# Kernel tuning notes

Measured on AMD Instinct MI355X. Metric: run time of the kernel, lower is better.

## Reference

```python
import jax, jax.numpy as jnp
import numpy as np


def conv1d(x, w, b, pad):
    # x: [N, Cin, L], w: [Cout, Cin, K] (torch OIH layout)
    out = jax.lax.conv_general_dilated(
        x, w, window_strides=(1,), padding=[(pad, pad)],
        dimension_numbers=("NCH", "OIH", "NCH"))
    return out + b[None, :, None]


def adaptive_avg_pool1d(x, out_size):
    # Faithful torch AdaptiveAvgPool1d: bin i covers [floor(i*L/D), ceil((i+1)*L/D))
    L = x.shape[-1]
    i = jnp.arange(out_size)
    starts = (i * L) // out_size
    ends = ((i + 1) * L + out_size - 1) // out_size
    zeros = jnp.zeros(x.shape[:-1] + (1,), dtype=x.dtype)
    cs = jnp.concatenate([zeros, jnp.cumsum(x, axis=-1)], axis=-1)
    counts = (ends - starts).astype(x.dtype)
    return (cs[..., ends] - cs[..., starts]) / counts


def setup_inputs() -> dict:
    key = jax.random.key(0)
    ks = jax.random.split(key, 12)
    B, C, T, D = 16, 64, 1024, 1024  # output_dim must equal seq_len (broadcast in forward)
    s = lambda fan: 1.0 / np.sqrt(fan)
    return {
        "eeg_data": jax.random.normal(ks[0], (B, C, T), jnp.float32),
        "filter_strength": jnp.ones((1,), jnp.float32),
        # spectral_attention params
        "aw1": jax.random.normal(ks[1], (32, 1, 64), jnp.float32) * s(64),
        "ab1": jnp.zeros((32,), jnp.float32),
        "aw2": jax.random.normal(ks[2], (64, 32, 32), jnp.float32) * s(32 * 32),
        "ab2": jnp.zeros((64,), jnp.float32),
        "aw3": jax.random.normal(ks[3], (1, 64, 1), jnp.float32) * s(64),
        "ab3": jnp.zeros((1,), jnp.float32),
        # feature_projection params
        "fw1": jax.random.normal(ks[4], (64, 1, 128), jnp.float32) * s(128),
        "fb1": jnp.zeros((64,), jnp.float32),
        "bn_g": jnp.ones((64,), jnp.float32),
        "bn_b": jnp.zeros((64,), jnp.float32),
        "bn_m": jnp.zeros((64,), jnp.float32),
        "bn_v": jnp.ones((64,), jnp.float32),
        "fw2": jax.random.normal(ks[5], (D, 64, 1), jnp.float32) * s(64),
        "fb2": jnp.zeros((D,), jnp.float32),
    }


def reference(eeg_data, filter_strength, aw1, ab1, aw2, ab2, aw3, ab3,
              fw1, fb1, bn_g, bn_b, bn_m, bn_v, fw2, fb2):
    B, C, T = eeg_data.shape
    D = fw2.shape[0]
    EPS = 1e-5
    # LearnableBandpassFilter: elementwise scale
    filt = eeg_data * filter_strength
    # spectral attention over channel-averaged signal
    ca = jnp.mean(filt, axis=1, keepdims=True)           # [B,1,T]
    a = jax.nn.relu(conv1d(ca, aw1, ab1, 32))            # [B,32,T+1]
    a = jax.nn.relu(conv1d(a, aw2, ab2, 16))             # [B,64,T+2]
    a = adaptive_avg_pool1d(a, D)                        # [B,64,D]
    attn = jax.nn.sigmoid(conv1d(a, aw3, ab3, 0))        # [B,1,D], D==T
    attended = filt * attn                               # [B,C,T]
    # feature_projection: shared weights over channels -> batch the python loop
    x = attended.reshape(B * C, 1, T)
    h = conv1d(x, fw1, fb1, 64)                          # [B*C,64,T+1]
    h = (h - bn_m[None, :, None]) * jax.lax.rsqrt(bn_v[None, :, None] + EPS)
    h = h * bn_g[None, :, None] + bn_b[None, :, None]
    h = jax.nn.relu(h)
    h = adaptive_avg_pool1d(h, D)                        # [B*C,64,D]
    h = conv1d(h, fw2, fb2, 0)                           # [B*C,D,D]
    feats = h.reshape(B, C, D, D).mean(axis=1)           # mean over channels
    return feats, attn[:, 0, :]
```

## Files before the change

### kernel.cpp

```cpp
#include <hip/hip_runtime.h>
#include <math.h>

#define Bn 16
#define Cn 64
#define Tn 1024
#define Dn 1024

#define CA_S   1088
#define CA_OFF 0
#define AT_OFF 17408
#define A2_S   1026
#define A2_OFF 599040
#define XS_U   (2*50176)
#define HS_S   1040
#define HS_OFF 2671616
#define HB_OFF 4801536

#define A1S_U  (2*HS_OFF)
#define HBT_U  (2*HB_OFF)
#define WFW2_U (HBT_U + 1048576)
#define WAW2_U (WFW2_U + 65536)
#define WFW1_U (WAW2_U + 65536)

typedef __attribute__((ext_vector_type(4))) float f32x4;
typedef __attribute__((ext_vector_type(8))) short bf16x8;
typedef __attribute__((ext_vector_type(4))) unsigned int u32x4;

static __device__ inline unsigned short f2bf(float x) {
  unsigned u = __builtin_bit_cast(unsigned, x);
  return (unsigned short)((u + 0x7fffu + ((u >> 16) & 1u)) >> 16);
}

__global__ void kI_init(const float* __restrict__ eeg, const float* __restrict__ fsp,
                        const float* __restrict__ aw2, const float* __restrict__ fw2,
                        const float* __restrict__ fw1, float* __restrict__ ws) {
  int bx = blockIdx.x, tid = threadIdx.x;
  if (bx < 64) {
    int b = bx >> 2, x = bx & 3;
    int t = x * 256 + tid;
    float s = 0.f;
#pragma unroll 8
    for (int c = 0; c < 64; ++c) s += eeg[(b * 64 + c) * 1024 + t];
    ws[CA_OFF + b * CA_S + 32 + t] = s * fsp[0] * (1.f / 64.f);
    if (x == 0 && tid < 32) ws[CA_OFF + b * CA_S + tid] = 0.f;
    if (x == 3 && tid >= 224) ws[CA_OFF + b * CA_S + 1056 + (tid - 224)] = 0.f;
    return;
  }
  int id = (bx - 64) * 256 + tid;
  if (id < 16384) {
    int e0 = id * 4;
    float4 f = *(const float4*)&aw2[e0];
    unsigned short* d = (unsigned short*)ws + WAW2_U + e0;
    d[0] = f2bf(f.x); d[1] = f2bf(f.y); d[2] = f2bf(f.z); d[3] = f2bf(f.w);
  } else if (id < 32768) {
    int e0 = (id - 16384) * 4;
    float4 f = *(const float4*)&fw2[e0];
    unsigned short* d = (unsigned short*)ws + WFW2_U + e0;
    d[0] = f2bf(f.x); d[1] = f2bf(f.y); d[2] = f2bf(f.z); d[3] = f2bf(f.w);
  } else if (id < 34816) {
    int e0 = (id - 32768) * 4;
    float4 f = *(const float4*)&fw1[e0];
    unsigned short* d = (unsigned short*)ws + WFW1_U + e0;
    d[0] = f2bf(f.x); d[1] = f2bf(f.y); d[2] = f2bf(f.z); d[3] = f2bf(f.w);
  }
}

__global__ void k2s_conv1(const float* __restrict__ aw1, const float* __restrict__ ab1,
                          float* __restrict__ ws) {
  int row = blockIdx.x;
  int b = row >> 5, o = row & 31;
  int tid = threadIdx.x;
  __shared__ unsigned short xl[1232];
  for (int i = tid; i < 1232; i += 256)
    if (i < 16 || i >= 1041) xl[i] = 0;
  const float* cab = ws + CA_OFF + b * CA_S;
  float bias = ab1[o];
  for (int t = tid; t < 1025; t += 256) {
    float acc = bias;
#pragma unroll 8
    for (int k = 0; k < 64; ++k) acc += aw1[o * 64 + k] * cab[t + k];
    xl[16 + t] = f2bf(fmaxf(acc, 0.f));
  }
  __syncthreads();
  unsigned short* a1s = (unsigned short*)ws + A1S_U;
  for (int q = tid; q < 608; q += 256) {
    int s = q / 152, mm = q % 152;
    int e = mm * 8;
    unsigned a0 = xl[e + s + 0], a1 = xl[e + s + 1], a2 = xl[e + s + 2], a3 = xl[e + s + 3];
    unsigned a4 = xl[e + s + 4], a5 = xl[e + s + 5], a6 = xl[e + s + 6], a7 = xl[e + s + 7];
    uint4 v;
    v.x = a0 | (a1 << 16); v.y = a2 | (a3 << 16); v.z = a4 | (a5 << 16); v.w = a6 | (a7 << 16);
    *(uint4*)&a1s[(s * 512 + row) * 1216 + e] = v;
  }
}

__global__ __launch_bounds__(256) void k3_mfma(const float* __restrict__ ab2,
                                               float* __restrict__ ws) {
  int t0 = blockIdx.x * 64, b = blockIdx.y, oh = blockIdx.z;
  int tid = threadIdx.x, l = tid & 63, w = tid >> 6;
  __shared__ unsigned short wlds[16 * 1032];
  __shared__ unsigned short xlds[32 * 4 * 104];
  const unsigned short* wb = (const unsigned short*)ws + WAW2_U;
  const unsigned short* a1s = (const unsigned short*)ws + A1S_U;
#pragma unroll
  for (int r = 0; r < 8; ++r) {
    int idx = tid + r * 256;
    int o = idx >> 7, j = idx & 127;
    *(uint4*)&wlds[o * 1032 + j * 8] = *(const uint4*)&wb[(oh * 16 + o) * 1024 + j * 8];
  }
#pragma unroll
  for (int r = 0; r < 6; ++r) {
    int idx = tid + r * 256;
    int i = idx / 48, rem = idx % 48, s = rem / 12, mm = rem % 12;
    *(uint4*)&xlds[(i * 4 + s) * 104 + mm * 8] =
        *(const uint4*)&a1s[(s * 512 + b * 32 + i) * 1216 + t0 + mm * 8];
  }
  __syncthreads();
  int m = l & 15, q = l >> 4;
  int A0 = w * 16 + m + q * 8;
  int xoffb = (A0 & 3) * 104 + (A0 & ~3);
  f32x4 acc = (f32x4){0.f, 0.f, 0.f, 0.f};
  for (int i = 0; i < 32; ++i) {
    const uint2* p = (const uint2*)&xlds[i * 416 + xoffb];
    uint2 lo = p[0], hi = p[1];
    u32x4 bb; bb.x = lo.x; bb.y = lo.y; bb.z = hi.x; bb.w = hi.y;
    u32x4 a = *(const u32x4*)&wlds[m * 1032 + i * 32 + q * 8];
    acc = __builtin_amdgcn_mfma_f32_16x16x32_bf16(
        __builtin_bit_cast(bf16x8, a), __builtin_bit_cast(bf16x8, bb), acc, 0, 0, 0);
  }
  int t = t0 + w * 16 + m;
  if (t < 1026) {
#pragma unroll
    for (int r = 0; r < 4; ++r) {
      int o = oh * 16 + q * 4 + r;
      ws[A2_OFF + (b * 64 + o) * A2_S + t] = fmaxf(acc[r] + ab2[o], 0.f);
    }
  }
}

__global__ void k4_attn(const float* __restrict__ aw3, const float* __restrict__ ab3,
                        float* __restrict__ ws, float* __restrict__ out) {
  int b = blockIdx.y, t = blockIdx.x * 256 + threadIdx.x;
  int s = t + (t >= 512 ? 1 : 0);
  float acc = 0.f;
#pragma unroll 8
  for (int i = 0; i < 64; ++i) {
    const float* row = ws + A2_OFF + (b * 64 + i) * A2_S;
    acc += aw3[i] * (row[s] + row[s + 1]);
  }
  float a = 1.f / (1.f + expf(-(acc * 0.5f + ab3[0])));
  ws[AT_OFF + b * 1024 + t] = a;
  out[16777216 + b * 1024 + t] = a;
}

__global__ void k4b_xs(const float* __restrict__ eeg, const float* __restrict__ fsp,
                       float* __restrict__ ws) {
  int bc = blockIdx.x;
  int b = bc >> 6;
  int tid = threadIdx.x;
  __shared__ unsigned short xsl[1288];
  float fs = fsp[0];
  for (int i = tid; i < 1288; i += 256) {
    int j = i - 64;
    float v = 0.f;
    if (j >= 0 && j < 1024) v = eeg[bc * 1024 + j] * fs * ws[AT_OFF + b * 1024 + j];
    xsl[i] = f2bf(v);
  }
  __syncthreads();
  unsigned short* xsg = (unsigned short*)ws + XS_U;
  for (int q = tid; q < 640; q += 256) {
    int s = q / 160, m = q % 160, e = m * 8;
    uint4 v;
    unsigned a0 = xsl[e + s + 0], a1 = xsl[e + s + 1], a2 = xsl[e + s + 2], a3 = xsl[e + s + 3];
    unsigned a4 = xsl[e + s + 4], a5 = xsl[e + s + 5], a6 = xsl[e + s + 6], a7 = xsl[e + s + 7];
    v.x = a0 | (a1 << 16); v.y = a2 | (a3 << 16); v.z = a4 | (a5 << 16); v.w = a6 | (a7 << 16);
    *(uint4*)&xsg[(s * 1024 + bc) * 1280 + e] = v;
  }
}

__global__ __launch_bounds__(256, 3) void k5_mfma(
    const float* __restrict__ fb1,
    const float* __restrict__ bng, const float* __restrict__ bnb,
    const float* __restrict__ bnm, const float* __restrict__ bnv,
    float* __restrict__ ws) {
  int t0 = blockIdx.x * 64, b = blockIdx.y, g2 = blockIdx.z;
  int tid = threadIdx.x, l = tid & 63, w = tid >> 6;
  __shared__ unsigned short xlds[32 * 4 * 200];
  const unsigned short* wbf = (const unsigned short*)ws + WFW1_U;
  const unsigned short* xsg = (const unsigned short*)ws + XS_U;
#pragma unroll
  for (int r = 0; r < 12; ++r) {
    int q = tid + r * 256;
    int ch = q / 96, rem = q % 96, s = rem / 24, m = rem % 24;
    int c = g2 * 32 + ch;
    uint4 v = *(const uint4*)&xsg[((s * 1024) + b * 64 + c) * 1280 + t0 + m * 8];
    *(uint4*)&xlds[(ch * 4 + s) * 200 + m * 8] = v;
  }
  u32x4 wf[4][4];
#pragma unroll
  for (int mt = 0; mt < 4; ++mt)
#pragma unroll
    for (int ks = 0; ks < 4; ++ks)
      wf[mt][ks] = *(const u32x4*)&wbf[(mt * 16 + (l & 15)) * 128 + ks * 32 + (l >> 4) * 8];
  int row0 = (l >> 4) * 4;
  float scv[4][4], shv[4][4];
#pragma unroll
  for (int mt = 0; mt < 4; ++mt)
#pragma unroll
    for (int r = 0; r < 4; ++r) {
      int o = mt * 16 + row0 + r;
      float s = bng[o] * rsqrtf(bnv[o] + 1e-5f);
      scv[mt][r] = s;
      shv[mt][r] = (fb1[o] - bnm[o]) * s + bnb[o];
    }
  int xoff[4];
#pragma unroll
  for (int ks = 0; ks < 4; ++ks) {
    int A0 = (l & 15) + ks * 32 + (l >> 4) * 8;
    int s = A0 & 3, e = A0 & ~3;
    xoff[ks] = s * 200 + w * 16 + e;
  }
  __syncthreads();
  f32x4 acc[4];
#pragma unroll
  for (int mt = 0; mt < 4; ++mt) acc[mt] = (f32x4){0.f, 0.f, 0.f, 0.f};
  for (int ch = 0; ch < 32; ++ch) {
    u32x4 bf[4];
#pragma unroll
    for (int ks = 0; ks < 4; ++ks) {
      const uint2* p = (const uint2*)&xlds[ch * 800 + xoff[ks]];
      uint2 lo = p[0], hi = p[1];
      u32x4 bb; bb.x = lo.x; bb.y = lo.y; bb.z = hi.x; bb.w = hi.y;
      bf[ks] = bb;
    }
#pragma unroll
    for (int mt = 0; mt < 4; ++mt) {
      f32x4 c = (f32x4){0.f, 0.f, 0.f, 0.f};
#pragma unroll
      for (int ks = 0; ks < 4; ++ks)
        c = __builtin_amdgcn_mfma_f32_16x16x32_bf16(
            __builtin_bit_cast(bf16x8, wf[mt][ks]),
            __builtin_bit_cast(bf16x8, bf[ks]), c, 0, 0, 0);
#pragma unroll
      for (int r = 0; r < 4; ++r)
        acc[mt][r] += fmaxf(c[r] * scv[mt][r] + shv[mt][r], 0.f);
    }
  }
  int t = t0 + w * 16 + (l & 15);
  if (t < 1025) {
#pragma unroll
    for (int mt = 0; mt < 4; ++mt)
#pragma unroll
      for (int r = 0; r < 4; ++r)
        ws[HS_OFF + (((g2 * 16 + b) * 64) + mt * 16 + row0 + r) * HS_S + t] = acc[mt][r];
  }
}

__global__ void k5b_t(float* __restrict__ ws) {
  int tt = blockIdx.x, b = blockIdx.y;
  int tid = threadIdx.x;
  __shared__ unsigned short tr[64 * 80];
  int k = tid >> 2, q = tid & 3;
  const float* r0 = ws + HS_OFF + ((0 + b) * 64 + k) * HS_S + tt * 64;
  const float* r1 = ws + HS_OFF + ((16 + b) * 64 + k) * HS_S + tt * 64;
#pragma unroll
  for (int j = 0; j < 16; ++j) {
    int tl = q * 16 + j;
    float v = r0[tl] + r0[tl + 1] + r1[tl] + r1[tl + 1];
    tr[tl * 80 + k] = f2bf(v * (1.f / 128.f));
  }
  __syncthreads();
  unsigned short* hbT = (unsigned short*)ws + HBT_U;
#pragma unroll
  for (int r = 0; r < 2; ++r) {
    int idx = tid + r * 256;
    int tl = idx >> 3, j = idx & 7;
    uint4 v = *(uint4*)&tr[tl * 80 + j * 8];
    *(uint4*)&hbT[(b * 1024 + tt * 64 + tl) * 64 + j * 8] = v;
  }
}

__global__ __launch_bounds__(256) void k6_mfma(const float* __restrict__ fb2,
                                               float* __restrict__ ws,
                                               float* __restrict__ out) {
  int tt = blockIdx.x, dt = blockIdx.y, b = blockIdx.z;
  int tid = threadIdx.x, l = tid & 63, w = tid >> 6;
  int wd = w >> 1, wt = w & 1;
  __shared__ unsigned short wA[64 * 80], xB[64 * 80];
  const unsigned short* w2 = (const unsigned short*)ws + WFW2_U;
  const unsigned short* hbT = (const unsigned short*)ws + HBT_U;
#pragma unroll
  for (int r = 0; r < 2; ++r) {
    int idx = tid + r * 256;
    int row = idx >> 3, j = idx & 7;
    *(uint4*)&wA[row * 80 + j * 8] = *(const uint4*)&w2[(dt * 64 + row) * 64 + j * 8];
    *(uint4*)&xB[row * 80 + j * 8] = *(const uint4*)&hbT[(b * 1024 + tt * 64 + row) * 64 + j * 8];
  }
  __syncthreads();
  int m = l & 15, q = l >> 4;
  f32x4 acc[2][2];
#pragma unroll
  for (int mt = 0; mt < 2; ++mt)
#pragma unroll
    for (int nt = 0; nt < 2; ++nt) acc[mt][nt] = (f32x4){0.f, 0.f, 0.f, 0.f};
#pragma unroll
  for (int ks = 0; ks < 2; ++ks) {
    u32x4 a[2], bb[2];
#pragma unroll
    for (int mt = 0; mt < 2; ++mt)
      a[mt] = *(const u32x4*)&wA[(wd * 32 + mt * 16 + m) * 80 + ks * 32 + q * 8];
#pragma unroll
    for (int nt = 0; nt < 2; ++nt)
      bb[nt] = *(const u32x4*)&xB[(wt * 32 + nt * 16 + m) * 80 + ks * 32 + q * 8];
#pragma unroll
    for (int mt = 0; mt < 2; ++mt)
#pragma unroll
      for (int nt = 0; nt < 2; ++nt)
        acc[mt][nt] = __builtin_amdgcn_mfma_f32_16x16x32_bf16(
            __builtin_bit_cast(bf16x8, a[mt]), __builtin_bit_cast(bf16x8, bb[nt]),
            acc[mt][nt], 0, 0, 0);
  }
#pragma unroll
  for (int mt = 0; mt < 2; ++mt) {
#pragma unroll
    for (int r = 0; r < 4; ++r) {
      int d = dt * 64 + wd * 32 + mt * 16 + q * 4 + r;
      float bias = fb2[d];
#pragma unroll
      for (int nt = 0; nt < 2; ++nt) {
        int t = tt * 64 + wt * 32 + nt * 16 + m;
        out[(b * 1024 + d) * 1024 + t] = acc[mt][nt][r] + bias;
      }
    }
  }
}

extern "C" void kernel_launch(void* const* d_in, const int* in_sizes, int n_in,
                              void* d_out, int out_size, void* d_ws, size_t ws_size,
                              hipStream_t stream) {
  const float* eeg = (const float*)d_in[0];
  const float* fsp = (const float*)d_in[1];
  const float* aw1 = (const float*)d_in[2];
  const float* ab1 = (const float*)d_in[3];
  const float* aw2 = (const float*)d_in[4];
  const float* ab2 = (const float*)d_in[5];
  const float* aw3 = (const float*)d_in[6];
  const float* ab3 = (const float*)d_in[7];
  const float* fw1 = (const float*)d_in[8];
  const float* fb1 = (const float*)d_in[9];
  const float* bng = (const float*)d_in[10];
  const float* bnb = (const float*)d_in[11];
  const float* bnm = (const float*)d_in[12];
  const float* bnv = (const float*)d_in[13];
  const float* fw2 = (const float*)d_in[14];
  const float* fb2 = (const float*)d_in[15];
  float* out = (float*)d_out;
  float* ws = (float*)d_ws;

  hipLaunchKernelGGL(kI_init, dim3(200), dim3(256), 0, stream, eeg, fsp, aw2, fw2, fw1, ws);
  hipLaunchKernelGGL(k2s_conv1, dim3(512), dim3(256), 0, stream, aw1, ab1, ws);
  hipLaunchKernelGGL(k3_mfma, dim3(17, 16, 4), dim3(256), 0, stream, ab2, ws);
  hipLaunchKernelGGL(k4_attn, dim3(4, 16), dim3(256), 0, stream, aw3, ab3, ws, out);
  hipLaunchKernelGGL(k4b_xs, dim3(1024), dim3(256), 0, stream, eeg, fsp, ws);
  hipLaunchKernelGGL(k5_mfma, dim3(17, 16, 2), dim3(256), 0, stream,
                     fb1, bng, bnb, bnm, bnv, ws);
  hipLaunchKernelGGL(k5b_t, dim3(16, 16), dim3(256), 0, stream, ws);
  hipLaunchKernelGGL(k6_mfma, dim3(16, 16, 16), dim3(256), 0, stream, fb2, ws, out);
}
```

Baseline: 178.3 us.

## Fuse pooling/transpose into final GEMM kernel and enlarge tiles to 128x128

Removes the separate k5b_t kernel that pooled and transposed the feature projection into bf16. k6_mfma now reads the fp32 hs buffer directly, pools adjacent pairs across the two half-channel partial sums, and writes the transposed bf16 tile into shared memory. The output tile grows from 64x64 to 128x128 per block, with 16 accumulators per wave. This saves one launch and the hbT round trip through memory. In exchange, each hs element is recomputed by the 8 d-tiles, and register pressure rises.

```diff
diff --git a/kernel.cpp b/kernel.cpp
--- a/kernel.cpp
+++ b/kernel.cpp
@@ -256,79 +256,69 @@
   }
 }
 
-__global__ void k5b_t(float* __restrict__ ws) {
-  int tt = blockIdx.x, b = blockIdx.y;
-  int tid = threadIdx.x;
-  __shared__ unsigned short tr[64 * 80];
-  int k = tid >> 2, q = tid & 3;
-  const float* r0 = ws + HS_OFF + ((0 + b) * 64 + k) * HS_S + tt * 64;
-  const float* r1 = ws + HS_OFF + ((16 + b) * 64 + k) * HS_S + tt * 64;
-#pragma unroll
-  for (int j = 0; j < 16; ++j) {
-    int tl = q * 16 + j;
-    float v = r0[tl] + r0[tl + 1] + r1[tl] + r1[tl + 1];
-    tr[tl * 80 + k] = f2bf(v * (1.f / 128.f));
-  }
-  __syncthreads();
-  unsigned short* hbT = (unsigned short*)ws + HBT_U;
-#pragma unroll
-  for (int r = 0; r < 2; ++r) {
-    int idx = tid + r * 256;
-    int tl = idx >> 3, j = idx & 7;
-    uint4 v = *(uint4*)&tr[tl * 80 + j * 8];
-    *(uint4*)&hbT[(b * 1024 + tt * 64 + tl) * 64 + j * 8] = v;
-  }
-}
-
-__global__ __launch_bounds__(256) void k6_mfma(const float* __restrict__ fb2,
-                                               float* __restrict__ ws,
-                                               float* __restrict__ out) {
+__global__ __launch_bounds__(256, 4) void k6_mfma(const float* __restrict__ fb2,
+                                                  float* __restrict__ ws,
+                                                  float* __restrict__ out) {
   int tt = blockIdx.x, dt = blockIdx.y, b = blockIdx.z;
   int tid = threadIdx.x, l = tid & 63, w = tid >> 6;
   int wd = w >> 1, wt = w & 1;
-  __shared__ unsigned short wA[64 * 80], xB[64 * 80];
+  __shared__ unsigned short wA[128 * 72];
+  __shared__ unsigned short xB[128 * 72];
   const unsigned short* w2 = (const unsigned short*)ws + WFW2_U;
-  const unsigned short* hbT = (const unsigned short*)ws + HBT_U;
-#pragma unroll
-  for (int r = 0; r < 2; ++r) {
+#pragma unroll
+  for (int r = 0; r < 4; ++r) {
     int idx = tid + r * 256;
     int row = idx >> 3, j = idx & 7;
-    *(uint4*)&wA[row * 80 + j * 8] = *(const uint4*)&w2[(dt * 64 + row) * 64 + j * 8];
-    *(uint4*)&xB[row * 80 + j * 8] = *(const uint4*)&hbT[(b * 1024 + tt * 64 + row) * 64 + j * 8];
-  }
-  __syncthreads();
-  int m = l & 15, q = l >> 4;
-  f32x4 acc[2][2];
-#pragma unroll
-  for (int mt = 0; mt < 2; ++mt)
-#pragma unroll
-    for (int nt = 0; nt < 2; ++nt) acc[mt][nt] = (f32x4){0.f, 0.f, 0.f, 0.f};
+    *(uint4*)&wA[row * 72 + j * 8] = *(const uint4*)&w2[(dt * 128 + row) * 64 + j * 8];
+  }
+  {
+    int k = tid >> 2, q = tid & 3;
+    const float* r0 = ws + HS_OFF + ((0 + b) * 64 + k) * HS_S + tt * 128 + q * 32;
+    const float* r1 = ws + HS_OFF + ((16 + b) * 64 + k) * HS_S + tt * 128 + q * 32;
+#pragma unroll
+    for (int jj = 0; jj < 8; ++jj) {
+      float4 p0 = *(const float4*)&r0[jj * 4];
+      float4 p1 = *(const float4*)&r1[jj * 4];
+      float n0 = r0[jj * 4 + 4], n1 = r1[jj * 4 + 4];
+      int tl = q * 32 + jj * 4;
+      xB[(tl + 0) * 72 + k] = f2bf((p0.x + p0.y + p1.x + p1.y) * (1.f / 128.f));
+      xB[(tl + 1) * 72 + k] = f2bf((p0.y + p0.z + p1.y + p1.z) * (1.f / 128.f));
+      xB[(tl + 2) * 72 + k] = f2bf((p0.z + p0.w + p1.z + p1.w) * (1.f / 128.f));
+      xB[(tl + 3) * 72 + k] = f2bf((p0.w + n0 + p1.w + n1) * (1.f / 128.f));
+    }
+  }
+  __syncthreads();
+  int m = l & 15, q8 = l >> 4;
+  f32x4 acc[4][4];
+#pragma unroll
+  for (int mt = 0; mt < 4; ++mt)
+#pragma unroll
+    for (int nt = 0; nt < 4; ++nt) acc[mt][nt] = (f32x4){0.f, 0.f, 0.f, 0.f};
 #pragma unroll
   for (int ks = 0; ks < 2; ++ks) {
-    u32x4 a[2], bb[2];
-#pragma unroll
-    for (int mt = 0; mt < 2; ++mt)
-      a[mt] = *(const u32x4*)&wA[(wd * 32 + mt * 16 + m) * 80 + ks * 32 + q * 8];
-#pragma unroll
-    for (int nt = 0; nt < 2; ++nt)
-      bb[nt] = *(const u32x4*)&xB[(wt * 32 + nt * 16 + m) * 80 + ks * 32 + q * 8];
-#pragma unroll
-    for (int mt = 0; mt < 2; ++mt)
-#pragma unroll
-      for (int nt = 0; nt < 2; ++nt)
+    u32x4 a[4];
+#pragma unroll
+    for (int mt = 0; mt < 4; ++mt)
+      a[mt] = *(const u32x4*)&wA[(wd * 64 + mt * 16 + m) * 72 + ks * 32 + q8 * 8];
+#pragma unroll
+    for (int nt = 0; nt < 4; ++nt) {
+      u32x4 bb = *(const u32x4*)&xB[(wt * 64 + nt * 16 + m) * 72 + ks * 32 + q8 * 8];
+#pragma unroll
+      for (int mt = 0; mt < 4; ++mt)
         acc[mt][nt] = __builtin_amdgcn_mfma_f32_16x16x32_bf16(
-            __builtin_bit_cast(bf16x8, a[mt]), __builtin_bit_cast(bf16x8, bb[nt]),
+            __builtin_bit_cast(bf16x8, a[mt]), __builtin_bit_cast(bf16x8, bb),
             acc[mt][nt], 0, 0, 0);
-  }
-#pragma unroll
-  for (int mt = 0; mt < 2; ++mt) {
+    }
+  }
+#pragma unroll
+  for (int mt = 0; mt < 4; ++mt) {
 #pragma unroll
     for (int r = 0; r < 4; ++r) {
-      int d = dt * 64 + wd * 32 + mt * 16 + q * 4 + r;
+      int d = dt * 128 + wd * 64 + mt * 16 + q8 * 4 + r;
       float bias = fb2[d];
 #pragma unroll
-      for (int nt = 0; nt < 2; ++nt) {
-        int t = tt * 64 + wt * 32 + nt * 16 + m;
+      for (int nt = 0; nt < 4; ++nt) {
+        int t = tt * 128 + wt * 64 + nt * 16 + m;
         out[(b * 1024 + d) * 1024 + t] = acc[mt][nt][r] + bias;
       }
     }
@@ -364,6 +354,5 @@
   hipLaunchKernelGGL(k4b_xs, dim3(1024), dim3(256), 0, stream, eeg, fsp, ws);
   hipLaunchKernelGGL(k5_mfma, dim3(17, 16, 2), dim3(256), 0, stream,
                      fb1, bng, bnb, bnm, bnv, ws);
-  hipLaunchKernelGGL(k5b_t, dim3(16, 16), dim3(256), 0, stream, ws);
-  hipLaunchKernelGGL(k6_mfma, dim3(16, 16, 16), dim3(256), 0, stream, fb2, ws, out);
-}
+  hipLaunchKernelGGL(k6_mfma, dim3(8, 8, 16), dim3(256), 0, stream, fb2, ws, out);
+}
```

After: 185.2 us. 3.8% more time.

## Fuse pooling-transpose into final GEMM and store conv features as bf16

Applied to the files above, without the earlier changes.

k5_mfma now writes its partial-sum features as scaled bf16 rather than fp32, and the separate k5b_t pooling/transpose kernel is removed. k6_mfma rebuilds its B tile by reading the bf16 partials, doing the adjacent-pair pooling sum and transpose directly into shared memory. This saves one kernel launch and halves the intermediate write/read traffic. The cost is redundant pooling work, since each of the 16 dt blocks recomputes the same tile. There is also an extra bf16 rounding step before pooling, which adds precision error.

```diff
diff --git a/kernel.cpp b/kernel.cpp
--- a/kernel.cpp
+++ b/kernel.cpp
@@ -11,12 +11,12 @@
 #define AT_OFF 17408
 #define A2_S   1026
 #define A2_OFF 599040
-#define XS_U   (2*50176)
-#define HS_S   1040
 #define HS_OFF 2671616
 #define HB_OFF 4801536
 
+#define XS_U   (2*50176)
 #define A1S_U  (2*HS_OFF)
+#define HSB_U  A1S_U
 #define HBT_U  (2*HB_OFF)
 #define WFW2_U (HBT_U + 1048576)
 #define WAW2_U (WFW2_U + 65536)
@@ -29,6 +29,10 @@
 static __device__ inline unsigned short f2bf(float x) {
   unsigned u = __builtin_bit_cast(unsigned, x);
   return (unsigned short)((u + 0x7fffu + ((u >> 16) & 1u)) >> 16);
+}
+static __device__ inline float bf2f(unsigned short h) {
+  unsigned u = ((unsigned)h) << 16;
+  return __builtin_bit_cast(float, u);
 }
 
 __global__ void kI_init(const float* __restrict__ eeg, const float* __restrict__ fsp,
@@ -247,36 +251,14 @@
     }
   }
   int t = t0 + w * 16 + (l & 15);
+  unsigned short* hsb = (unsigned short*)ws + HSB_U;
   if (t < 1025) {
 #pragma unroll
     for (int mt = 0; mt < 4; ++mt)
 #pragma unroll
       for (int r = 0; r < 4; ++r)
-        ws[HS_OFF + (((g2 * 16 + b) * 64) + mt * 16 + row0 + r) * HS_S + t] = acc[mt][r];
-  }
-}
-
-__global__ void k5b_t(float* __restrict__ ws) {
-  int tt = blockIdx.x, b = blockIdx.y;
-  int tid = threadIdx.x;
-  __shared__ unsigned short tr[64 * 80];
-  int k = tid >> 2, q = tid & 3;
-  const float* r0 = ws + HS_OFF + ((0 + b) * 64 + k) * HS_S + tt * 64;
-  const float* r1 = ws + HS_OFF + ((16 + b) * 64 + k) * HS_S + tt * 64;
-#pragma unroll
-  for (int j = 0; j < 16; ++j) {
-    int tl = q * 16 + j;
-    float v = r0[tl] + r0[tl + 1] + r1[tl] + r1[tl + 1];
-    tr[tl * 80 + k] = f2bf(v * (1.f / 128.f));
-  }
-  __syncthreads();
-  unsigned short* hbT = (unsigned short*)ws + HBT_U;
-#pragma unroll
-  for (int r = 0; r < 2; ++r) {
-    int idx = tid + r * 256;
-    int tl = idx >> 3, j = idx & 7;
-    uint4 v = *(uint4*)&tr[tl * 80 + j * 8];
-    *(uint4*)&hbT[(b * 1024 + tt * 64 + tl) * 64 + j * 8] = v;
+        hsb[(((g2 * 16 + b) * 64) + mt * 16 + row0 + r) * 1040 + t] =
+            f2bf(acc[mt][r] * 0.0078125f);
   }
 }
 
@@ -288,13 +270,22 @@
   int wd = w >> 1, wt = w & 1;
   __shared__ unsigned short wA[64 * 80], xB[64 * 80];
   const unsigned short* w2 = (const unsigned short*)ws + WFW2_U;
-  const unsigned short* hbT = (const unsigned short*)ws + HBT_U;
+  const unsigned short* hsb = (const unsigned short*)ws + HSB_U;
 #pragma unroll
   for (int r = 0; r < 2; ++r) {
     int idx = tid + r * 256;
     int row = idx >> 3, j = idx & 7;
     *(uint4*)&wA[row * 80 + j * 8] = *(const uint4*)&w2[(dt * 64 + row) * 64 + j * 8];
-    *(uint4*)&xB[row * 80 + j * 8] = *(const uint4*)&hbT[(b * 1024 + tt * 64 + row) * 64 + j * 8];
+  }
+  {
+    int k = tid >> 2, q = tid & 3;
+    const unsigned short* h0 = hsb + ((0 + b) * 64 + k) * 1040 + tt * 64 + q * 16;
+    const unsigned short* h1 = hsb + ((16 + b) * 64 + k) * 1040 + tt * 64 + q * 16;
+#pragma unroll
+    for (int j = 0; j < 16; ++j) {
+      float v = bf2f(h0[j]) + bf2f(h0[j + 1]) + bf2f(h1[j]) + bf2f(h1[j + 1]);
+      xB[(q * 16 + j) * 80 + k] = f2bf(v);
+    }
   }
   __syncthreads();
   int m = l & 15, q = l >> 4;
@@ -364,6 +355,5 @@
   hipLaunchKernelGGL(k4b_xs, dim3(1024), dim3(256), 0, stream, eeg, fsp, ws);
   hipLaunchKernelGGL(k5_mfma, dim3(17, 16, 2), dim3(256), 0, stream,
                      fb1, bng, bnb, bnm, bnv, ws);
-  hipLaunchKernelGGL(k5b_t, dim3(16, 16), dim3(256), 0, stream, ws);
   hipLaunchKernelGGL(k6_mfma, dim3(16, 16, 16), dim3(256), 0, stream, fb2, ws, out);
 }
```

Measured after the change: 181.2 us. Within noise of the previous version (+1.6%).
